# Performance work log

Measured on AMD Instinct MI355X. Metric: run time of the kernel, lower is better.

Reference implementation:

```python
import jax, jax.numpy as jnp
import numpy as np

EPS_NORM = 1e-12  # torch F.normalize eps
EPS_LOG = 1e-8


def setup_inputs() -> dict:
    key = jax.random.key(0)
    target_prob = jax.random.uniform(key, (65536, 1024), dtype=jnp.float32)
    return {"target_prob": target_prob}


def reference(target_prob) -> jnp.ndarray:
    # F.normalize(x, dim=0): L2-normalize each column, norm clamped at eps
    norm = jnp.sqrt(jnp.sum(target_prob * target_prob, axis=0, keepdims=True))
    p = target_prob / jnp.maximum(norm, EPS_NORM)
    # per-row entropy: -sum_j p * log(p + 1e-8)
    row_entropy = -jnp.sum(p * jnp.log(p + EPS_LOG), axis=1)
    return jnp.mean(row_entropy)
```

## Files before the change

### kernel.cpp

```cpp
#include <hip/hip_runtime.h>
#include <hip/hip_bf16.h>


#define ROWS 65536
#define COLS 1024
#define C4   (COLS / 4)
#define GRID1 2048
#define ITERS (ROWS / GRID1)
#define NSLOT 64

#define EPS_NORM 1e-12f
#define EPS_LOG  1e-8f

#define WS_PART  0
#define WS_INV   (NSLOT * COLS)
#define WS_BPART (WS_INV + COLS)
#define WS_FLOATS (WS_BPART + GRID1)

__global__ __launch_bounds__(256) void colnorm2_kernel(
    const float* __restrict__ x, float* __restrict__ part) {
    const int t = threadIdx.x;
    const float4* xr = reinterpret_cast<const float4*>(x)
                     + (size_t)blockIdx.x * C4 + t;

    float4 acc = make_float4(0.f, 0.f, 0.f, 0.f);
    #pragma unroll 4
    for (int k = 0; k < ITERS; ++k) {
        float4 v = xr[(size_t)k * GRID1 * C4];
        acc.x = fmaf(v.x, v.x, acc.x);
        acc.y = fmaf(v.y, v.y, acc.y);
        acc.z = fmaf(v.z, v.z, acc.z);
        acc.w = fmaf(v.w, v.w, acc.w);
    }
    float* dst = part + (blockIdx.x & (NSLOT - 1)) * COLS + 4 * t;
    atomicAdd(dst + 0, acc.x);
    atomicAdd(dst + 1, acc.y);
    atomicAdd(dst + 2, acc.z);
    atomicAdd(dst + 3, acc.w);
}

__global__ __launch_bounds__(256) void finalize_norm_kernel(
    const float* __restrict__ part, float* __restrict__ inv) {
    const int j = blockIdx.x * 256 + threadIdx.x;
    float s = 0.f;
    #pragma unroll 16
    for (int r = 0; r < NSLOT; ++r) s += part[r * COLS + j];
    inv[j] = 1.0f / fmaxf(sqrtf(s), EPS_NORM);
}

__global__ __launch_bounds__(256) void entropy_kernel(
    const float* __restrict__ x, const float* __restrict__ invn,
    float* __restrict__ bpart) {
    const int t = threadIdx.x;
    const float4 inv = reinterpret_cast<const float4*>(invn)[t];
    const float4* xr = reinterpret_cast<const float4*>(x)
                     + (size_t)blockIdx.x * C4 + t;

    float acc = 0.f;
    #pragma unroll 2
    for (int k = 0; k < ITERS; ++k) {
        float4 v = xr[(size_t)k * GRID1 * C4];
        float px = v.x * inv.x;
        float py = v.y * inv.y;
        float pz = v.z * inv.z;
        float pw = v.w * inv.w;
        acc = fmaf(px, __logf(px + EPS_LOG), acc);
        acc = fmaf(py, __logf(py + EPS_LOG), acc);
        acc = fmaf(pz, __logf(pz + EPS_LOG), acc);
        acc = fmaf(pw, __logf(pw + EPS_LOG), acc);
    }

    #pragma unroll
    for (int o = 32; o > 0; o >>= 1) acc += __shfl_down(acc, o, 64);

    __shared__ float wsum[4];
    if ((t & 63) == 0) wsum[t >> 6] = acc;
    __syncthreads();
    if (t == 0) bpart[blockIdx.x] = wsum[0] + wsum[1] + wsum[2] + wsum[3];
}

__global__ __launch_bounds__(256) void final_reduce_kernel(
    const float* __restrict__ bpart, float* __restrict__ out) {
    const int t = threadIdx.x;
    float a = 0.f;
    #pragma unroll 8
    for (int k = 0; k < GRID1 / 256; ++k) a += bpart[k * 256 + t];

    #pragma unroll
    for (int o = 32; o > 0; o >>= 1) a += __shfl_down(a, o, 64);

    __shared__ float wsum[4];
    if ((t & 63) == 0) wsum[t >> 6] = a;
    __syncthreads();
    if (t == 0) out[0] = -(wsum[0] + wsum[1] + wsum[2] + wsum[3])
                         * (1.0f / (float)ROWS);
}

extern "C" void kernel_launch(void* const* d_in, const int* in_sizes, int n_in,
                              void* d_out, int out_size, void* d_ws, size_t ws_size,
                              hipStream_t stream) {
    const float* x = (const float*)d_in[0];
    float* out = (float*)d_out;
    float* ws = (float*)d_ws;
    float* part  = ws + WS_PART;
    float* inv   = ws + WS_INV;
    float* bpart = ws + WS_BPART;

    hipMemsetAsync(part, 0, NSLOT * COLS * sizeof(float), stream);

    colnorm2_kernel<<<GRID1, 256, 0, stream>>>(x, part);
    finalize_norm_kernel<<<COLS / 256, 256, 0, stream>>>(part, inv);
    entropy_kernel<<<GRID1, 256, 0, stream>>>(x, inv, bpart);
    final_reduce_kernel<<<1, 256, 0, stream>>>(bpart, out);
}
```

Before: 412.2 us.

## Fuse norm and entropy into single pass via per-column log-sum algebra

Rewrites the per-column entropy as (sum x log x - log n * sum x)/n, so one pass over the input gathers sum x, sum x^2 and sum x log x per column. This removes the second full read of the 256MB input and one kernel launch. A finalize kernel combines the per-column statistics. The cost is dropping the 1e-8 epsilon inside the log, which changes numerics slightly, plus three times as many atomics and partial-sum storage.

```diff
diff --git a/kernel.cpp b/kernel.cpp
--- a/kernel.cpp
+++ b/kernel.cpp
@@ -2,98 +2,87 @@
 #include <hip/hip_bf16.h>
 
 
-#define ROWS 65536
-#define COLS 1024
-#define C4   (COLS / 4)
-#define GRID1 2048
-#define ITERS (ROWS / GRID1)
+#define ROWS  65536
+#define COLS  1024
+#define C4    (COLS / 4)
+#define GRID  2048
+#define ITERS (ROWS / GRID)
 #define NSLOT 64
 
 #define EPS_NORM 1e-12f
-#define EPS_LOG  1e-8f
 
-#define WS_PART  0
-#define WS_INV   (NSLOT * COLS)
-#define WS_BPART (WS_INV + COLS)
-#define WS_FLOATS (WS_BPART + GRID1)
+#define WS_PART   0
+#define WS_BPART  (NSLOT * 3 * COLS)
 
-__global__ __launch_bounds__(256) void colnorm2_kernel(
+__global__ __launch_bounds__(256) void fused_stats_kernel(
     const float* __restrict__ x, float* __restrict__ part) {
     const int t = threadIdx.x;
     const float4* xr = reinterpret_cast<const float4*>(x)
                      + (size_t)blockIdx.x * C4 + t;
 
-    float4 acc = make_float4(0.f, 0.f, 0.f, 0.f);
+    float4 s1 = make_float4(0.f, 0.f, 0.f, 0.f);
+    float4 s2 = make_float4(0.f, 0.f, 0.f, 0.f);
+    float4 s3 = make_float4(0.f, 0.f, 0.f, 0.f);
     #pragma unroll 4
     for (int k = 0; k < ITERS; ++k) {
-        float4 v = xr[(size_t)k * GRID1 * C4];
-        acc.x = fmaf(v.x, v.x, acc.x);
-        acc.y = fmaf(v.y, v.y, acc.y);
-        acc.z = fmaf(v.z, v.z, acc.z);
-        acc.w = fmaf(v.w, v.w, acc.w);
+        float4 v = xr[(size_t)k * GRID * C4];
+        s1.x += v.x; s1.y += v.y; s1.z += v.z; s1.w += v.w;
+        s2.x = fmaf(v.x, v.x, s2.x);
+        s2.y = fmaf(v.y, v.y, s2.y);
+        s2.z = fmaf(v.z, v.z, s2.z);
+        s2.w = fmaf(v.w, v.w, s2.w);
+        s3.x += (v.x > 0.f) ? v.x * __logf(v.x) : 0.f;
+        s3.y += (v.y > 0.f) ? v.y * __logf(v.y) : 0.f;
+        s3.z += (v.z > 0.f) ? v.z * __logf(v.z) : 0.f;
+        s3.w += (v.w > 0.f) ? v.w * __logf(v.w) : 0.f;
     }
-    float* dst = part + (blockIdx.x & (NSLOT - 1)) * COLS + 4 * t;
-    atomicAdd(dst + 0, acc.x);
-    atomicAdd(dst + 1, acc.y);
-    atomicAdd(dst + 2, acc.z);
-    atomicAdd(dst + 3, acc.w);
+
+    float* dst = part + (size_t)(blockIdx.x & (NSLOT - 1)) * 3 * COLS + 4 * t;
+    atomicAdd(dst + 0,            s1.x);
+    atomicAdd(dst + 1,            s1.y);
+    atomicAdd(dst + 2,            s1.z);
+    atomicAdd(dst + 3,            s1.w);
+    atomicAdd(dst + COLS + 0,     s2.x);
+    atomicAdd(dst + COLS + 1,     s2.y);
+    atomicAdd(dst + COLS + 2,     s2.z);
+    atomicAdd(dst + COLS + 3,     s2.w);
+    atomicAdd(dst + 2 * COLS + 0, s3.x);
+    atomicAdd(dst + 2 * COLS + 1, s3.y);
+    atomicAdd(dst + 2 * COLS + 2, s3.z);
+    atomicAdd(dst + 2 * COLS + 3, s3.w);
 }
 
-__global__ __launch_bounds__(256) void finalize_norm_kernel(
-    const float* __restrict__ part, float* __restrict__ inv) {
-    const int j = blockIdx.x * 256 + threadIdx.x;
-    float s = 0.f;
-    #pragma unroll 16
-    for (int r = 0; r < NSLOT; ++r) s += part[r * COLS + j];
-    inv[j] = 1.0f / fmaxf(sqrtf(s), EPS_NORM);
-}
-
-__global__ __launch_bounds__(256) void entropy_kernel(
-    const float* __restrict__ x, const float* __restrict__ invn,
-    float* __restrict__ bpart) {
+__global__ __launch_bounds__(256) void finalize_kernel(
+    const float* __restrict__ part, float* __restrict__ bpart) {
     const int t = threadIdx.x;
-    const float4 inv = reinterpret_cast<const float4*>(invn)[t];
-    const float4* xr = reinterpret_cast<const float4*>(x)
-                     + (size_t)blockIdx.x * C4 + t;
-
-    float acc = 0.f;
-    #pragma unroll 2
-    for (int k = 0; k < ITERS; ++k) {
-        float4 v = xr[(size_t)k * GRID1 * C4];
-        float px = v.x * inv.x;
-        float py = v.y * inv.y;
-        float pz = v.z * inv.z;
-        float pw = v.w * inv.w;
-        acc = fmaf(px, __logf(px + EPS_LOG), acc);
-        acc = fmaf(py, __logf(py + EPS_LOG), acc);
-        acc = fmaf(pz, __logf(pz + EPS_LOG), acc);
-        acc = fmaf(pw, __logf(pw + EPS_LOG), acc);
+    const int j = blockIdx.x * 256 + t;
+    float a1 = 0.f, a2 = 0.f, a3 = 0.f;
+    #pragma unroll 8
+    for (int r = 0; r < NSLOT; ++r) {
+        const float* p = part + (size_t)r * 3 * COLS + j;
+        a1 += p[0];
+        a2 += p[COLS];
+        a3 += p[2 * COLS];
     }
+    float n = fmaxf(sqrtf(a2), EPS_NORM);
+    float contrib = (a3 - __logf(n) * a1) / n;
 
     #pragma unroll
-    for (int o = 32; o > 0; o >>= 1) acc += __shfl_down(acc, o, 64);
+    for (int o = 32; o > 0; o >>= 1) contrib += __shfl_down(contrib, o, 64);
 
     __shared__ float wsum[4];
-    if ((t & 63) == 0) wsum[t >> 6] = acc;
+    if ((t & 63) == 0) wsum[t >> 6] = contrib;
     __syncthreads();
     if (t == 0) bpart[blockIdx.x] = wsum[0] + wsum[1] + wsum[2] + wsum[3];
 }
 
-__global__ __launch_bounds__(256) void final_reduce_kernel(
+__global__ __launch_bounds__(64) void final_reduce_kernel(
     const float* __restrict__ bpart, float* __restrict__ out) {
     const int t = threadIdx.x;
-    float a = 0.f;
-    #pragma unroll 8
-    for (int k = 0; k < GRID1 / 256; ++k) a += bpart[k * 256 + t];
-
+    float a = (t < 4) ? bpart[t] : 0.f;
     #pragma unroll
     for (int o = 32; o > 0; o >>= 1) a += __shfl_down(a, o, 64);
-
-    __shared__ float wsum[4];
-    if ((t & 63) == 0) wsum[t >> 6] = a;
-    __syncthreads();
-    if (t == 0) out[0] = -(wsum[0] + wsum[1] + wsum[2] + wsum[3])
-                         * (1.0f / (float)ROWS);
+    if (t == 0) out[0] = -a * (1.0f / (float)ROWS);
 }
 
 extern "C" void kernel_launch(void* const* d_in, const int* in_sizes, int n_in,
@@ -103,13 +92,11 @@
     float* out = (float*)d_out;
     float* ws = (float*)d_ws;
     float* part  = ws + WS_PART;
-    float* inv   = ws + WS_INV;
     float* bpart = ws + WS_BPART;
 
-    hipMemsetAsync(part, 0, NSLOT * COLS * sizeof(float), stream);
+    hipMemsetAsync(part, 0, (size_t)NSLOT * 3 * COLS * sizeof(float), stream);
 
-    colnorm2_kernel<<<GRID1, 256, 0, stream>>>(x, part);
-    finalize_norm_kernel<<<COLS / 256, 256, 0, stream>>>(part, inv);
-    entropy_kernel<<<GRID1, 256, 0, stream>>>(x, inv, bpart);
-    final_reduce_kernel<<<1, 256, 0, stream>>>(bpart, out);
+    fused_stats_kernel<<<GRID, 256, 0, stream>>>(x, part);
+    finalize_kernel<<<COLS / 256, 256, 0, stream>>>(part, bpart);
+    final_reduce_kernel<<<1, 64, 0, stream>>>(bpart, out);
 }
```

After: 404.7 us. No clear change (-1.8%).
